# Optimization experiments

Measured on AMD Instinct MI355X. Metric: run time of the kernel, lower is better.

Reference implementation:

```python
import jax, jax.numpy as jnp
import numpy as np

TOP_K = 2
EPS = float(np.finfo(np.float64).eps)  # combine() clamps zeros to np.finfo(float).eps


def setup_inputs() -> dict:
    key = jax.random.key(0)
    ks = jax.random.split(key, 6)
    B, D, H, O, E = 2048, 1024, 2048, 512, 8
    return {
        "x": jax.random.normal(ks[0], (B, D), dtype=jnp.float32),
        "w_gate": jax.random.normal(ks[1], (D, E), dtype=jnp.float32) * 0.02,
        "fc1_w": jax.random.normal(ks[2], (E, D, H), dtype=jnp.float32) * 0.02,
        "fc1_b": jax.random.normal(ks[3], (E, H), dtype=jnp.float32) * 0.02,
        "fc2_w": jax.random.normal(ks[4], (E, H, O), dtype=jnp.float32) * 0.02,
        "fc2_b": jax.random.normal(ks[5], (E, O), dtype=jnp.float32) * 0.02,
    }


def _gates(x, w_gate):
    # Noisy top-k gating in eval mode (no noise): clean logits -> top-k -> softmax over top-k -> scatter.
    logits = x @ w_gate                              # [B, E]
    top_logits, top_idx = jax.lax.top_k(logits, TOP_K)  # [B, K]
    top_gates = jax.nn.softmax(top_logits, axis=-1)      # 'softmax' gating over selected experts
    B = x.shape[0]
    gates = jnp.zeros(logits.shape, logits.dtype)
    gates = gates.at[jnp.arange(B)[:, None], top_idx].set(top_gates)
    return gates                                      # [B, E], zero for non-selected experts


def reference(x, w_gate, fc1_w, fc1_b, fc2_w, fc2_b):
    gates = _gates(x, w_gate)                         # [B, E]
    # Dense-equivalent of SparseDispatcher: non-selected experts have gate 0,
    # so weighting by gates reproduces dispatch/expert/combine exactly.
    h = jax.nn.gelu(jnp.einsum('bd,edh->ebh', x, fc1_w) + fc1_b[:, None, :],
                    approximate=False)                # [E, B, H]
    logp = jax.nn.log_softmax(jnp.einsum('ebh,eho->ebo', h, fc2_w) + fc2_b[:, None, :],
                              axis=-1)                # [E, B, O] (MLP ends with LogSoftmax)
    # combine: sum_e gates[b,e] * exp(logp_e[b]), clamp zeros to eps, then log
    combined = jnp.einsum('ebo,be->bo', jnp.exp(logp), gates)  # [B, O]
    combined = jnp.where(combined == 0, jnp.asarray(EPS, combined.dtype), combined)
    return jnp.log(combined)
```

## Files before the change

### kernel.cpp

```cpp
#include <hip/hip_runtime.h>
#include <stdint.h>

#define Bn 2048
#define Dn 1024
#define Hn 2048
#define On 512
#define En 8

typedef __bf16 bf16x8 __attribute__((ext_vector_type(8)));
typedef float f32x4 __attribute__((ext_vector_type(4)));
typedef unsigned short ushort_t;
typedef ushort_t ushort8v __attribute__((ext_vector_type(8)));

__device__ __forceinline__ ushort_t f2bf(float v) {
  union { float f; uint32_t u; } a; a.f = v;
  uint32_t u = a.u;
  return (ushort_t)((u + 0x7fffu + ((u >> 16) & 1u)) >> 16);
}

__device__ __forceinline__ void gload16(const void* g, void* l) {
  __builtin_amdgcn_global_load_lds((const uint32_t*)g, (uint32_t*)l, 16, 0, 0);
}

__global__ void init_kernel(int* counts, int* cursors) {
  int t = threadIdx.x;
  if (t < En) { counts[t] = 0; cursors[t] = 0; }
}

#define NB_G (Bn / 8)
#define NB_T1 ((Dn / 64) * (Hn / 64) * En)
#define NB_T2 ((Hn / 64) * (On / 64) * En)

__device__ __forceinline__ void tcast64(const float* __restrict__ inp, ushort_t* __restrict__ outp,
                                        int R, int C, int r0, int c0, float* tile ) {
  int t = threadIdx.x;
  int rr = t >> 4;
  int cc4 = (t & 15) * 4;
#pragma unroll
  for (int j = 0; j < 4; j++) {
    float4 v = *(const float4*)&inp[(size_t)(r0 + j * 16 + rr) * C + c0 + cc4];
    float* tp = &tile[(j * 16 + rr) * 65 + cc4];
    tp[0] = v.x; tp[1] = v.y; tp[2] = v.z; tp[3] = v.w;
  }
  __syncthreads();
  int orow = t >> 2, g = t & 3;
  ushort8v o0, o1;
#pragma unroll
  for (int i = 0; i < 8; i++) o0[i] = f2bf(tile[(g * 16 + i) * 65 + orow]);
#pragma unroll
  for (int i = 0; i < 8; i++) o1[i] = f2bf(tile[(g * 16 + 8 + i) * 65 + orow]);
  ushort_t* op = &outp[(size_t)(c0 + orow) * R + r0 + g * 16];
  *(ushort8v*)op = o0;
  *(ushort8v*)(op + 8) = o1;
}

__global__ __launch_bounds__(256) void prep_kernel(
    const float* __restrict__ x, const float* __restrict__ wg,
    const float* __restrict__ fc1w, const float* __restrict__ fc2w,
    ushort_t* __restrict__ x_bf, ushort_t* __restrict__ w1t, ushort_t* __restrict__ w2t,
    int* __restrict__ top_idx, float* __restrict__ gates, int* __restrict__ counts) {
  __shared__ float smem[En * Dn];
  __shared__ int lcnt[En];
  int bid = blockIdx.x;
  int t = threadIdx.x;

  if (bid < NB_G) {
    float* wgs = smem;
    for (int i = t; i < Dn * En; i += 256) {
      int d = i >> 3, e = i & 7;
      wgs[e * Dn + d] = wg[i];
    }
    if (t < En) lcnt[t] = 0;
    __syncthreads();
    int w = t >> 6, lane = t & 63;
#pragma unroll
    for (int r = 0; r < 2; r++) {
      int b = bid * 8 + w * 2 + r;
      const float* xr = x + (size_t)b * Dn;
      ushort_t* xo = x_bf + (size_t)b * Dn;
      float xv[16];
#pragma unroll
      for (int j = 0; j < 16; j++) xv[j] = xr[lane + j * 64];
      float acc[En];
#pragma unroll
      for (int e = 0; e < En; e++) acc[e] = 0.f;
#pragma unroll
      for (int j = 0; j < 16; j++) {
        int d = lane + j * 64;
        xo[d] = f2bf(xv[j]);
#pragma unroll
        for (int e = 0; e < En; e++) acc[e] += xv[j] * wgs[e * Dn + d];
      }
#pragma unroll
      for (int off = 32; off; off >>= 1) {
#pragma unroll
        for (int e = 0; e < En; e++) acc[e] += __shfl_down(acc[e], off);
      }
      if (lane == 0) {
        float best = -1e30f, second = -1e30f; int bi = 0, si = 0;
#pragma unroll
        for (int e = 0; e < En; e++) {
          float l = acc[e];
          if (l > best) { second = best; si = bi; best = l; bi = e; }
          else if (l > second) { second = l; si = e; }
        }
        float e1 = expf(second - best);
        float inv = 1.f / (1.f + e1);
        top_idx[2 * b] = bi; top_idx[2 * b + 1] = si;
        gates[2 * b] = inv;  gates[2 * b + 1] = e1 * inv;
        atomicAdd(&lcnt[bi], 1);
        atomicAdd(&lcnt[si], 1);
      }
    }
    __syncthreads();
    if (t < En) {
      int c = lcnt[t];
      if (c) atomicAdd(&counts[t], c);
    }
  } else if (bid < NB_G + NB_T1) {
    int idx = bid - NB_G;
    constexpr int TPE = (Dn / 64) * (Hn / 64);
    int z = idx / TPE, rem = idx % TPE;
    int r0 = (rem / (Hn / 64)) * 64, c0 = (rem % (Hn / 64)) * 64;
    tcast64(fc1w + (size_t)z * Dn * Hn, w1t + (size_t)z * Dn * Hn, Dn, Hn, r0, c0, smem);
  } else {
    int idx = bid - NB_G - NB_T1;
    constexpr int TPE = (Hn / 64) * (On / 64);
    int z = idx / TPE, rem = idx % TPE;
    int r0 = (rem / (On / 64)) * 64, c0 = (rem % (On / 64)) * 64;
    tcast64(fc2w + (size_t)z * Hn * On, w2t + (size_t)z * Hn * On, Hn, On, r0, c0, smem);
  }
}

__global__ void offsets_kernel(const int* counts, int* offsets, int* cursors) {
  if (threadIdx.x == 0) {
    int s = 0;
    for (int e = 0; e < En; e++) { offsets[e] = s; s += counts[e]; }
  }
  if (threadIdx.x < En) cursors[threadIdx.x] = 0;
}

__global__ void assign_kernel(const int* __restrict__ top_idx, const int* __restrict__ offsets,
                              int* cursors, int* __restrict__ s2r, int* __restrict__ r2s) {
  int b = blockIdx.x * 256 + threadIdx.x;
  if (b >= Bn) return;
#pragma unroll
  for (int k = 0; k < 2; k++) {
    int e = top_idx[2 * b + k];
    int pos = atomicAdd(&cursors[e], 1);
    int slot = offsets[e] + pos;
    s2r[slot] = b;
    r2s[2 * b + k] = slot;
  }
}

template <bool GATHER, bool FC1, int N, int K, int SPLITK>
__global__ __launch_bounds__(256, 8) void moe_gemm_kernel(
    const ushort_t* __restrict__ A, const ushort_t* __restrict__ WT,
    const float* __restrict__ bias, const int* __restrict__ offsets,
    const int* __restrict__ counts, const int* __restrict__ s2r,
    ushort_t* __restrict__ outH, float* __restrict__ outL, float* __restrict__ outL2) {
  constexpr int NBL = N / 64;
  constexpr int KS = K / SPLITK;
  constexpr int NT = KS / 64;
  int e = blockIdx.z;
  int cnt = counts[e];
  int rb = blockIdx.y;
  if (rb * 64 >= cnt) return;
  int base = offsets[e];
  int ks = blockIdx.x / NBL;
  int nb = (blockIdx.x % NBL) * 64;
  int k0 = ks * KS;
  __shared__ __align__(16) ushort_t As[64 * 64];
  __shared__ __align__(16) ushort_t Bs[64 * 64];
  int t = threadIdx.x;
  int lane = t & 63, w = t >> 6;
  int wr = w >> 1, wc = w & 1;

  int srow = t >> 3;
  int scol = ((t & 7) ^ (srow & 7)) * 8;

  const ushort_t* aptr[2];
#pragma unroll
  for (int i = 0; i < 2; i++) {
    int lr = rb * 64 + i * 32 + srow;
    int lrc = lr < cnt ? lr : cnt - 1;
    int slot = base + lrc;
    int row = GATHER ? s2r[slot] : slot;
    aptr[i] = A + (size_t)row * K + k0 + scol;
  }
  const ushort_t* bptr = WT + ((size_t)e * N + nb + srow) * K + k0 + scol;

  f32x4 zero = {0.f, 0.f, 0.f, 0.f};
  f32x4 acc[2][2];
#pragma unroll
  for (int m = 0; m < 2; m++)
#pragma unroll
    for (int n = 0; n < 2; n++) acc[m][n] = zero;

  int a_r = wr * 32 + (lane & 15);
  int b_r = wc * 32 + (lane & 15);
  int axor = lane & 7;
  int c16 = lane >> 4;

  for (int kt = 0; kt < NT; kt++) {
#pragma unroll
    for (int i = 0; i < 2; i++) gload16(aptr[i] + kt * 64, &As[i * 2048 + t * 8]);
#pragma unroll
    for (int i = 0; i < 2; i++)
      gload16(bptr + (size_t)i * 32 * K + kt * 64, &Bs[i * 2048 + t * 8]);
    __syncthreads();
#pragma unroll
    for (int kk = 0; kk < 2; kk++) {
      bf16x8 af[2], bfr[2];
#pragma unroll
      for (int m = 0; m < 2; m++)
        af[m] = *(const bf16x8*)((const char*)As + (a_r + m * 16) * 128 +
                                 (((kk * 4 + c16) ^ axor) << 4));
#pragma unroll
      for (int n = 0; n < 2; n++)
        bfr[n] = *(const bf16x8*)((const char*)Bs + (b_r + n * 16) * 128 +
                                  (((kk * 4 + c16) ^ axor) << 4));
#pragma unroll
      for (int m = 0; m < 2; m++)
#pragma unroll
        for (int n = 0; n < 2; n++)
          acc[m][n] = __builtin_amdgcn_mfma_f32_16x16x32_bf16(af[m], bfr[n], acc[m][n], 0, 0, 0);
    }
    __syncthreads();
  }

  float* dst = (SPLITK > 1 && ks > 0) ? (outL2 + (size_t)(ks - 1) * (2 * Bn * On)) : outL;
  int lr0 = rb * 64 + wr * 32;
#pragma unroll
  for (int m = 0; m < 2; m++) {
#pragma unroll
    for (int i = 0; i < 4; i++) {
      int lr = lr0 + m * 16 + (lane >> 4) * 4 + i;
      if (lr < cnt) {
        int slot = base + lr;
#pragma unroll
        for (int n = 0; n < 2; n++) {
          int col = nb + wc * 32 + n * 16 + (lane & 15);
          float v = acc[m][n][i] + (ks == 0 ? bias[e * N + col] : 0.f);
          if (FC1) {
            float g = 0.5f * v * (1.0f + erff(v * 0.70710678118654752f));
            outH[(size_t)slot * N + col] = f2bf(g);
          } else {
            dst[(size_t)slot * N + col] = v;
          }
        }
      }
    }
  }
}

__device__ __forceinline__ float blk_reduce(float v, bool ismax) {
  __shared__ float sbuf[4];
  int lane = threadIdx.x & 63, w = threadIdx.x >> 6;
#pragma unroll
  for (int off = 32; off; off >>= 1) {
    float o = __shfl_down(v, off);
    v = ismax ? fmaxf(v, o) : (v + o);
  }
  __syncthreads();
  if (lane == 0) sbuf[w] = v;
  __syncthreads();
  float r = sbuf[0];
#pragma unroll
  for (int i = 1; i < 4; i++) r = ismax ? fmaxf(r, sbuf[i]) : (r + sbuf[i]);
  return r;
}

__global__ void combine_kernel(const float* __restrict__ l2a, const float* __restrict__ l2b,
                               const int* __restrict__ r2s, const float* __restrict__ gates,
                               float* __restrict__ out) {
  int b = blockIdx.x, t = threadIdx.x;
  float c0 = 0.f, c1 = 0.f;
#pragma unroll
  for (int k = 0; k < 2; k++) {
    int slot = r2s[2 * b + k];
    float g = gates[2 * b + k];
    const float* lp0 = l2a + (size_t)slot * On;
    const float* lp1 = l2b + (size_t)slot * On;
    float v0 = lp0[t] + lp1[t];
    float v1 = lp0[t + 256] + lp1[t + 256];
    float m = blk_reduce(fmaxf(v0, v1), true);
    float s = blk_reduce(expf(v0 - m) + expf(v1 - m), false);
    float lse = m + logf(s);
    c0 += g * expf(v0 - lse);
    c1 += g * expf(v1 - lse);
  }
  const float EPSv = 2.220446049250313e-16f;
  out[(size_t)b * On + t] = logf(fmaxf(c0, EPSv));
  out[(size_t)b * On + t + 256] = logf(fmaxf(c1, EPSv));
}

extern "C" void kernel_launch(void* const* d_in, const int* in_sizes, int n_in,
                              void* d_out, int out_size, void* d_ws, size_t ws_size,
                              hipStream_t stream) {
  const float* x = (const float*)d_in[0];
  const float* wgate = (const float*)d_in[1];
  const float* fc1w = (const float*)d_in[2];
  const float* fc1b = (const float*)d_in[3];
  const float* fc2w = (const float*)d_in[4];
  const float* fc2b = (const float*)d_in[5];
  float* out = (float*)d_out;

  char* ws = (char*)d_ws;
  size_t o = 0;
  ushort_t* x_bf = (ushort_t*)(ws + o); o += (size_t)Bn * Dn * 2;
  ushort_t* w1t  = (ushort_t*)(ws + o); o += (size_t)En * Hn * Dn * 2;
  ushort_t* w2t  = (ushort_t*)(ws + o); o += (size_t)En * On * Hn * 2;
  ushort_t* hbuf = (ushort_t*)(ws + o); o += (size_t)2 * Bn * Hn * 2;
  float* l2buf   = (float*)(ws + o);    o += (size_t)2 * Bn * On * 4;
  int* top_idx   = (int*)(ws + o);      o += (size_t)Bn * 2 * 4;
  float* gates   = (float*)(ws + o);    o += (size_t)Bn * 2 * 4;
  int* r2s       = (int*)(ws + o);      o += (size_t)Bn * 2 * 4;
  int* s2r       = (int*)(ws + o);      o += (size_t)2 * Bn * 4;
  int* counts    = (int*)(ws + o);      o += 64;
  int* offsets   = (int*)(ws + o);      o += 64;
  int* cursors   = (int*)(ws + o);      o += 64;
  float* l2buf1  = (float*)w1t;

  hipLaunchKernelGGL(init_kernel, dim3(1), dim3(64), 0, stream, counts, cursors);
  hipLaunchKernelGGL(prep_kernel, dim3(NB_G + NB_T1 + NB_T2), dim3(256), 0, stream,
                     x, wgate, fc1w, fc2w, x_bf, w1t, w2t, top_idx, gates, counts);
  hipLaunchKernelGGL(offsets_kernel, dim3(1), dim3(64), 0, stream, counts, offsets, cursors);
  hipLaunchKernelGGL(assign_kernel, dim3(Bn / 256), dim3(256), 0, stream,
                     top_idx, offsets, cursors, s2r, r2s);
  hipLaunchKernelGGL((moe_gemm_kernel<true, true, Hn, Dn, 1>), dim3(Hn / 64, 32, En), dim3(256),
                     0, stream, x_bf, w1t, fc1b, offsets, counts, s2r, hbuf, (float*)nullptr,
                     (float*)nullptr);
  hipLaunchKernelGGL((moe_gemm_kernel<false, false, On, Hn, 2>), dim3((On / 64) * 2, 32, En),
                     dim3(256), 0, stream, hbuf, w2t, fc2b, offsets, counts, s2r,
                     (ushort_t*)nullptr, l2buf, l2buf1);
  hipLaunchKernelGGL(combine_kernel, dim3(Bn), dim3(256), 0, stream, l2buf, l2buf1, r2s, gates, out);
}
```

Before: 131.6 us.

## Run fc1 expert GEMM in FP8 with scaled weights and separate x cast

New measurement: 124.9 us. 1.05x faster.

```diff
diff --git a/kernel.cpp b/kernel.cpp
--- a/kernel.cpp
+++ b/kernel.cpp
@@ -11,6 +11,7 @@
 typedef float f32x4 __attribute__((ext_vector_type(4)));
 typedef unsigned short ushort_t;
 typedef ushort_t ushort8v __attribute__((ext_vector_type(8)));
+typedef unsigned char u8;
 
 __device__ __forceinline__ ushort_t f2bf(float v) {
   union { float f; uint32_t u; } a; a.f = v;
@@ -22,20 +23,40 @@
   __builtin_amdgcn_global_load_lds((const uint32_t*)g, (uint32_t*)l, 16, 0, 0);
 }
 
+__device__ __forceinline__ int pk4_fp8(float a, float b, float c, float d) {
+  int w = __builtin_amdgcn_cvt_pk_fp8_f32(a, b, 0, false);
+  w = __builtin_amdgcn_cvt_pk_fp8_f32(c, d, w, true);
+  return w;
+}
+
 __global__ void init_kernel(int* counts, int* cursors) {
   int t = threadIdx.x;
   if (t < En) { counts[t] = 0; cursors[t] = 0; }
+}
+
+__global__ __launch_bounds__(256) void cast_x8_kernel(const float* __restrict__ in,
+                                                      u8* __restrict__ out) {
+  int i = blockIdx.x * 256 + threadIdx.x;
+  const float4* p = (const float4*)in + (size_t)i * 4;
+  float4 a = p[0], b = p[1], c = p[2], d = p[3];
+  int4 o;
+  o.x = pk4_fp8(a.x, a.y, a.z, a.w);
+  o.y = pk4_fp8(b.x, b.y, b.z, b.w);
+  o.z = pk4_fp8(c.x, c.y, c.z, c.w);
+  o.w = pk4_fp8(d.x, d.y, d.z, d.w);
+  *(int4*)(out + (size_t)i * 16) = o;
 }
 
 #define NB_G (Bn / 8)
 #define NB_T1 ((Dn / 64) * (Hn / 64) * En)
 #define NB_T2 ((Hn / 64) * (On / 64) * En)
-
-__device__ __forceinline__ void tcast64(const float* __restrict__ inp, ushort_t* __restrict__ outp,
-                                        int R, int C, int r0, int c0, float* tile ) {
-  int t = threadIdx.x;
-  int rr = t >> 4;
-  int cc4 = (t & 15) * 4;
+#define W1SCALE 64.0f
+
+__device__ __forceinline__ void tcast64_bf(const float* __restrict__ inp,
+                                           ushort_t* __restrict__ outp,
+                                           int R, int C, int r0, int c0, float* tile) {
+  int t = threadIdx.x;
+  int rr = t >> 4, cc4 = (t & 15) * 4;
 #pragma unroll
   for (int j = 0; j < 4; j++) {
     float4 v = *(const float4*)&inp[(size_t)(r0 + j * 16 + rr) * C + c0 + cc4];
@@ -54,10 +75,35 @@
   *(ushort8v*)(op + 8) = o1;
 }
 
+__device__ __forceinline__ void tcast64_f8(const float* __restrict__ inp,
+                                           u8* __restrict__ outp,
+                                           int R, int C, int r0, int c0, float* tile) {
+  int t = threadIdx.x;
+  int rr = t >> 4, cc4 = (t & 15) * 4;
+#pragma unroll
+  for (int j = 0; j < 4; j++) {
+    float4 v = *(const float4*)&inp[(size_t)(r0 + j * 16 + rr) * C + c0 + cc4];
+    float* tp = &tile[(j * 16 + rr) * 65 + cc4];
+    tp[0] = v.x; tp[1] = v.y; tp[2] = v.z; tp[3] = v.w;
+  }
+  __syncthreads();
+  int orow = t >> 2, g = t & 3;
+  int4 o;
+#pragma unroll
+  for (int q = 0; q < 4; q++) {
+    float v0 = tile[(g * 16 + q * 4 + 0) * 65 + orow] * W1SCALE;
+    float v1 = tile[(g * 16 + q * 4 + 1) * 65 + orow] * W1SCALE;
+    float v2 = tile[(g * 16 + q * 4 + 2) * 65 + orow] * W1SCALE;
+    float v3 = tile[(g * 16 + q * 4 + 3) * 65 + orow] * W1SCALE;
+    ((int*)&o)[q] = pk4_fp8(v0, v1, v2, v3);
+  }
+  *(int4*)&outp[(size_t)(c0 + orow) * R + r0 + g * 16] = o;
+}
+
 __global__ __launch_bounds__(256) void prep_kernel(
     const float* __restrict__ x, const float* __restrict__ wg,
     const float* __restrict__ fc1w, const float* __restrict__ fc2w,
-    ushort_t* __restrict__ x_bf, ushort_t* __restrict__ w1t, ushort_t* __restrict__ w2t,
+    u8* __restrict__ w1t8, ushort_t* __restrict__ w2t,
     int* __restrict__ top_idx, float* __restrict__ gates, int* __restrict__ counts) {
   __shared__ float smem[En * Dn];
   __shared__ int lcnt[En];
@@ -77,7 +123,6 @@
     for (int r = 0; r < 2; r++) {
       int b = bid * 8 + w * 2 + r;
       const float* xr = x + (size_t)b * Dn;
-      ushort_t* xo = x_bf + (size_t)b * Dn;
       float xv[16];
 #pragma unroll
       for (int j = 0; j < 16; j++) xv[j] = xr[lane + j * 64];
@@ -87,7 +132,6 @@
 #pragma unroll
       for (int j = 0; j < 16; j++) {
         int d = lane + j * 64;
-        xo[d] = f2bf(xv[j]);
 #pragma unroll
         for (int e = 0; e < En; e++) acc[e] += xv[j] * wgs[e * Dn + d];
       }
@@ -122,13 +166,13 @@
     constexpr int TPE = (Dn / 64) * (Hn / 64);
     int z = idx / TPE, rem = idx % TPE;
     int r0 = (rem / (Hn / 64)) * 64, c0 = (rem % (Hn / 64)) * 64;
-    tcast64(fc1w + (size_t)z * Dn * Hn, w1t + (size_t)z * Dn * Hn, Dn, Hn, r0, c0, smem);
+    tcast64_f8(fc1w + (size_t)z * Dn * Hn, w1t8 + (size_t)z * Dn * Hn, Dn, Hn, r0, c0, smem);
   } else {
     int idx = bid - NB_G - NB_T1;
     constexpr int TPE = (Hn / 64) * (On / 64);
     int z = idx / TPE, rem = idx % TPE;
     int r0 = (rem / (On / 64)) * 64, c0 = (rem % (On / 64)) * 64;
-    tcast64(fc2w + (size_t)z * Hn * On, w2t + (size_t)z * Hn * On, Hn, On, r0, c0, smem);
+    tcast64_bf(fc2w + (size_t)z * Hn * On, w2t + (size_t)z * Hn * On, Hn, On, r0, c0, smem);
   }
 }
 
@@ -154,12 +198,98 @@
   }
 }
 
-template <bool GATHER, bool FC1, int N, int K, int SPLITK>
-__global__ __launch_bounds__(256, 8) void moe_gemm_kernel(
+__global__ __launch_bounds__(256, 8) void fc1_fp8_kernel(
+    const u8* __restrict__ A, const u8* __restrict__ WT,
+    const float* __restrict__ bias, const int* __restrict__ offsets,
+    const int* __restrict__ counts, const int* __restrict__ s2r,
+    ushort_t* __restrict__ outH) {
+  constexpr int K = Dn;
+  constexpr int NT = K / 64;
+  int e = blockIdx.z;
+  int cnt = counts[e];
+  int rb = blockIdx.y;
+  if (rb * 64 >= cnt) return;
+  int base = offsets[e];
+  int nb = blockIdx.x * 64;
+  __shared__ __align__(16) u8 As[64 * 64];
+  __shared__ __align__(16) u8 Bs[64 * 64];
+  int t = threadIdx.x;
+  int lane = t & 63, w = t >> 6;
+  int wr = w >> 1, wc = w & 1;
+
+  int srow = t >> 2;
+  int sslot = (t & 3) ^ ((srow >> 1) & 3);
+  int scol = sslot * 16;
+
+  int lr = rb * 64 + srow;
+  int lrc = lr < cnt ? lr : cnt - 1;
+  const u8* aptr = A + (size_t)s2r[base + lrc] * K + scol;
+  const u8* bptr = WT + ((size_t)e * Hn + nb + srow) * K + scol;
+
+  f32x4 zero = {0.f, 0.f, 0.f, 0.f};
+  f32x4 acc[2][2];
+#pragma unroll
+  for (int m = 0; m < 2; m++)
+#pragma unroll
+    for (int n = 0; n < 2; n++) acc[m][n] = zero;
+
+  int a_r = wr * 32 + (lane & 15);
+  int b_r = wc * 32 + (lane & 15);
+  int rkey = ((lane & 15) >> 1) & 3;
+  int slb = (lane >> 4) >> 1;
+  int half = ((lane >> 4) & 1) * 8;
+
+  for (int kt = 0; kt < NT; kt++) {
+    gload16(aptr + kt * 64, &As[t * 16]);
+    gload16(bptr + kt * 64, &Bs[t * 16]);
+    __syncthreads();
+#pragma unroll
+    for (int kk = 0; kk < 2; kk++) {
+      long af[2], bfr[2];
+#pragma unroll
+      for (int m = 0; m < 2; m++)
+        af[m] = *(const long*)(As + (a_r + m * 16) * 64 +
+                               (((kk * 2 + slb) ^ rkey) << 4) + half);
+#pragma unroll
+      for (int n = 0; n < 2; n++)
+        bfr[n] = *(const long*)(Bs + (b_r + n * 16) * 64 +
+                                (((kk * 2 + slb) ^ rkey) << 4) + half);
+#pragma unroll
+      for (int m = 0; m < 2; m++)
+#pragma unroll
+        for (int n = 0; n < 2; n++)
+          acc[m][n] = __builtin_amdgcn_mfma_f32_16x16x32_fp8_fp8(af[m], bfr[n], acc[m][n], 0, 0, 0);
+    }
+    __syncthreads();
+  }
+
+  const float INV = 1.0f / W1SCALE;
+  int lr0 = rb * 64 + wr * 32;
+#pragma unroll
+  for (int m = 0; m < 2; m++) {
+#pragma unroll
+    for (int i = 0; i < 4; i++) {
+      int orow = lr0 + m * 16 + (lane >> 4) * 4 + i;
+      if (orow < cnt) {
+        int slot = base + orow;
+#pragma unroll
+        for (int n = 0; n < 2; n++) {
+          int col = nb + wc * 32 + n * 16 + (lane & 15);
+          float v = acc[m][n][i] * INV + bias[e * Hn + col];
+          float g = 0.5f * v * (1.0f + erff(v * 0.70710678118654752f));
+          outH[(size_t)slot * Hn + col] = f2bf(g);
+        }
+      }
+    }
+  }
+}
+
+template <int N, int K, int SPLITK>
+__global__ __launch_bounds__(256, 8) void fc2_gemm_kernel(
     const ushort_t* __restrict__ A, const ushort_t* __restrict__ WT,
     const float* __restrict__ bias, const int* __restrict__ offsets,
-    const int* __restrict__ counts, const int* __restrict__ s2r,
-    ushort_t* __restrict__ outH, float* __restrict__ outL, float* __restrict__ outL2) {
+    const int* __restrict__ counts,
+    float* __restrict__ outL, float* __restrict__ outL2) {
   constexpr int NBL = N / 64;
   constexpr int KS = K / SPLITK;
   constexpr int NT = KS / 64;
@@ -185,9 +315,7 @@
   for (int i = 0; i < 2; i++) {
     int lr = rb * 64 + i * 32 + srow;
     int lrc = lr < cnt ? lr : cnt - 1;
-    int slot = base + lrc;
-    int row = GATHER ? s2r[slot] : slot;
-    aptr[i] = A + (size_t)row * K + k0 + scol;
+    aptr[i] = A + (size_t)(base + lrc) * K + k0 + scol;
   }
   const ushort_t* bptr = WT + ((size_t)e * N + nb + srow) * K + k0 + scol;
 
@@ -230,7 +358,7 @@
     __syncthreads();
   }
 
-  float* dst = (SPLITK > 1 && ks > 0) ? (outL2 + (size_t)(ks - 1) * (2 * Bn * On)) : outL;
+  float* dst = (ks > 0) ? outL2 : outL;
   int lr0 = rb * 64 + wr * 32;
 #pragma unroll
   for (int m = 0; m < 2; m++) {
@@ -243,12 +371,7 @@
         for (int n = 0; n < 2; n++) {
           int col = nb + wc * 32 + n * 16 + (lane & 15);
           float v = acc[m][n][i] + (ks == 0 ? bias[e * N + col] : 0.f);
-          if (FC1) {
-            float g = 0.5f * v * (1.0f + erff(v * 0.70710678118654752f));
-            outH[(size_t)slot * N + col] = f2bf(g);
-          } else {
-            dst[(size_t)slot * N + col] = v;
-          }
+          dst[(size_t)slot * N + col] = v;
         }
       }
     }
@@ -309,8 +432,8 @@
 
   char* ws = (char*)d_ws;
   size_t o = 0;
-  ushort_t* x_bf = (ushort_t*)(ws + o); o += (size_t)Bn * Dn * 2;
-  ushort_t* w1t  = (ushort_t*)(ws + o); o += (size_t)En * Hn * Dn * 2;
+  u8* x_f8       = (u8*)(ws + o);       o += (size_t)Bn * Dn;
+  u8* w1t8       = (u8*)(ws + o);       o += (size_t)En * Hn * Dn;
   ushort_t* w2t  = (ushort_t*)(ws + o); o += (size_t)En * On * Hn * 2;
   ushort_t* hbuf = (ushort_t*)(ws + o); o += (size_t)2 * Bn * Hn * 2;
   float* l2buf   = (float*)(ws + o);    o += (size_t)2 * Bn * On * 4;
@@ -321,19 +444,18 @@
   int* counts    = (int*)(ws + o);      o += 64;
   int* offsets   = (int*)(ws + o);      o += 64;
   int* cursors   = (int*)(ws + o);      o += 64;
-  float* l2buf1  = (float*)w1t;
+  float* l2buf1  = (float*)w1t8;
 
   hipLaunchKernelGGL(init_kernel, dim3(1), dim3(64), 0, stream, counts, cursors);
+  hipLaunchKernelGGL(cast_x8_kernel, dim3(Bn * Dn / 16 / 256), dim3(256), 0, stream, x, x_f8);
   hipLaunchKernelGGL(prep_kernel, dim3(NB_G + NB_T1 + NB_T2), dim3(256), 0, stream,
-                     x, wgate, fc1w, fc2w, x_bf, w1t, w2t, top_idx, gates, counts);
+                     x, wgate, fc1w, fc2w, w1t8, w2t, top_idx, gates, counts);
   hipLaunchKernelGGL(offsets_kernel, dim3(1), dim3(64), 0, stream, counts, offsets, cursors);
   hipLaunchKernelGGL(assign_kernel, dim3(Bn / 256), dim3(256), 0, stream,
                      top_idx, offsets, cursors, s2r, r2s);
-  hipLaunchKernelGGL((moe_gemm_kernel<true, true, Hn, Dn, 1>), dim3(Hn / 64, 32, En), dim3(256),
-                     0, stream, x_bf, w1t, fc1b, offsets, counts, s2r, hbuf, (float*)nullptr,
-                     (float*)nullptr);
-  hipLaunchKernelGGL((moe_gemm_kernel<false, false, On, Hn, 2>), dim3((On / 64) * 2, 32, En),
-                     dim3(256), 0, stream, hbuf, w2t, fc2b, offsets, counts, s2r,
-                     (ushort_t*)nullptr, l2buf, l2buf1);
+  hipLaunchKernelGGL(fc1_fp8_kernel, dim3(Hn / 64, 32, En), dim3(256), 0, stream,
+                     x_f8, w1t8, fc1b, offsets, counts, s2r, hbuf);
+  hipLaunchKernelGGL((fc2_gemm_kernel<On, Hn, 2>), dim3((On / 64) * 2, 32, En), dim3(256),
+                     0, stream, hbuf, w2t, fc2b, offsets, counts, l2buf, l2buf1);
   hipLaunchKernelGGL(combine_kernel, dim3(Bn), dim3(256), 0, stream, l2buf, l2buf1, r2s, gates, out);
 }
```

## Switch expert GEMMs from bf16 to fp8 with scaled weights

Applied to the files above, without the earlier changes.

Measured after the change: 115.2 us. -12.4%, faster.

```diff
diff --git a/kernel.cpp b/kernel.cpp
--- a/kernel.cpp
+++ b/kernel.cpp
@@ -7,10 +7,9 @@
 #define On 512
 #define En 8
 
-typedef __bf16 bf16x8 __attribute__((ext_vector_type(8)));
 typedef float f32x4 __attribute__((ext_vector_type(4)));
 typedef unsigned short ushort_t;
-typedef ushort_t ushort8v __attribute__((ext_vector_type(8)));
+typedef unsigned char u8;
 
 __device__ __forceinline__ ushort_t f2bf(float v) {
   union { float f; uint32_t u; } a; a.f = v;
@@ -22,20 +21,45 @@
   __builtin_amdgcn_global_load_lds((const uint32_t*)g, (uint32_t*)l, 16, 0, 0);
 }
 
+__device__ __forceinline__ int pk4_fp8(float a, float b, float c, float d) {
+  int w = __builtin_amdgcn_cvt_pk_fp8_f32(a, b, 0, false);
+  w = __builtin_amdgcn_cvt_pk_fp8_f32(c, d, w, true);
+  return w;
+}
+
+__device__ __forceinline__ u8 f2fp8(float v) {
+  int w = __builtin_amdgcn_cvt_pk_fp8_f32(v, v, 0, false);
+  return (u8)(w & 0xff);
+}
+
 __global__ void init_kernel(int* counts, int* cursors) {
   int t = threadIdx.x;
   if (t < En) { counts[t] = 0; cursors[t] = 0; }
 }
 
+__global__ __launch_bounds__(256) void cast_x8_kernel(const float* __restrict__ in,
+                                                      u8* __restrict__ out) {
+  int i = blockIdx.x * 256 + threadIdx.x;
+  const float4* p = (const float4*)in + (size_t)i * 4;
+  float4 a = p[0], b = p[1], c = p[2], d = p[3];
+  int4 o;
+  o.x = pk4_fp8(a.x, a.y, a.z, a.w);
+  o.y = pk4_fp8(b.x, b.y, b.z, b.w);
+  o.z = pk4_fp8(c.x, c.y, c.z, c.w);
+  o.w = pk4_fp8(d.x, d.y, d.z, d.w);
+  *(int4*)(out + (size_t)i * 16) = o;
+}
+
 #define NB_G (Bn / 8)
 #define NB_T1 ((Dn / 64) * (Hn / 64) * En)
 #define NB_T2 ((Hn / 64) * (On / 64) * En)
-
-__device__ __forceinline__ void tcast64(const float* __restrict__ inp, ushort_t* __restrict__ outp,
-                                        int R, int C, int r0, int c0, float* tile ) {
+#define WSCALE 64.0f
+
+__device__ __forceinline__ void tcast64_f8(const float* __restrict__ inp,
+                                           u8* __restrict__ outp,
+                                           int R, int C, int r0, int c0, float* tile) {
   int t = threadIdx.x;
-  int rr = t >> 4;
-  int cc4 = (t & 15) * 4;
+  int rr = t >> 4, cc4 = (t & 15) * 4;
 #pragma unroll
   for (int j = 0; j < 4; j++) {
     float4 v = *(const float4*)&inp[(size_t)(r0 + j * 16 + rr) * C + c0 + cc4];
@@ -44,20 +68,22 @@
   }
   __syncthreads();
   int orow = t >> 2, g = t & 3;
-  ushort8v o0, o1;
-#pragma unroll
-  for (int i = 0; i < 8; i++) o0[i] = f2bf(tile[(g * 16 + i) * 65 + orow]);
-#pragma unroll
-  for (int i = 0; i < 8; i++) o1[i] = f2bf(tile[(g * 16 + 8 + i) * 65 + orow]);
-  ushort_t* op = &outp[(size_t)(c0 + orow) * R + r0 + g * 16];
-  *(ushort8v*)op = o0;
-  *(ushort8v*)(op + 8) = o1;
+  int4 o;
+#pragma unroll
+  for (int q = 0; q < 4; q++) {
+    float v0 = tile[(g * 16 + q * 4 + 0) * 65 + orow] * WSCALE;
+    float v1 = tile[(g * 16 + q * 4 + 1) * 65 + orow] * WSCALE;
+    float v2 = tile[(g * 16 + q * 4 + 2) * 65 + orow] * WSCALE;
+    float v3 = tile[(g * 16 + q * 4 + 3) * 65 + orow] * WSCALE;
+    ((int*)&o)[q] = pk4_fp8(v0, v1, v2, v3);
+  }
+  *(int4*)&outp[(size_t)(c0 + orow) * R + r0 + g * 16] = o;
 }
 
 __global__ __launch_bounds__(256) void prep_kernel(
     const float* __restrict__ x, const float* __restrict__ wg,
     const float* __restrict__ fc1w, const float* __restrict__ fc2w,
-    ushort_t* __restrict__ x_bf, ushort_t* __restrict__ w1t, ushort_t* __restrict__ w2t,
+    u8* __restrict__ w1t8, u8* __restrict__ w2t8,
     int* __restrict__ top_idx, float* __restrict__ gates, int* __restrict__ counts) {
   __shared__ float smem[En * Dn];
   __shared__ int lcnt[En];
@@ -77,7 +103,6 @@
     for (int r = 0; r < 2; r++) {
       int b = bid * 8 + w * 2 + r;
       const float* xr = x + (size_t)b * Dn;
-      ushort_t* xo = x_bf + (size_t)b * Dn;
       float xv[16];
 #pragma unroll
       for (int j = 0; j < 16; j++) xv[j] = xr[lane + j * 64];
@@ -87,7 +112,6 @@
 #pragma unroll
       for (int j = 0; j < 16; j++) {
         int d = lane + j * 64;
-        xo[d] = f2bf(xv[j]);
 #pragma unroll
         for (int e = 0; e < En; e++) acc[e] += xv[j] * wgs[e * Dn + d];
       }
@@ -122,13 +146,13 @@
     constexpr int TPE = (Dn / 64) * (Hn / 64);
     int z = idx / TPE, rem = idx % TPE;
     int r0 = (rem / (Hn / 64)) * 64, c0 = (rem % (Hn / 64)) * 64;
-    tcast64(fc1w + (size_t)z * Dn * Hn, w1t + (size_t)z * Dn * Hn, Dn, Hn, r0, c0, smem);
+    tcast64_f8(fc1w + (size_t)z * Dn * Hn, w1t8 + (size_t)z * Dn * Hn, Dn, Hn, r0, c0, smem);
   } else {
     int idx = bid - NB_G - NB_T1;
     constexpr int TPE = (Hn / 64) * (On / 64);
     int z = idx / TPE, rem = idx % TPE;
     int r0 = (rem / (On / 64)) * 64, c0 = (rem % (On / 64)) * 64;
-    tcast64(fc2w + (size_t)z * Hn * On, w2t + (size_t)z * Hn * On, Hn, On, r0, c0, smem);
+    tcast64_f8(fc2w + (size_t)z * Hn * On, w2t8 + (size_t)z * Hn * On, Hn, On, r0, c0, smem);
   }
 }
 
@@ -154,12 +178,12 @@
   }
 }
 
-template <bool GATHER, bool FC1, int N, int K, int SPLITK>
-__global__ __launch_bounds__(256, 8) void moe_gemm_kernel(
-    const ushort_t* __restrict__ A, const ushort_t* __restrict__ WT,
+template <bool FC1, int N, int K, int SPLITK>
+__global__ __launch_bounds__(256, 8) void fp8_gemm_kernel(
+    const u8* __restrict__ A, const u8* __restrict__ WT,
     const float* __restrict__ bias, const int* __restrict__ offsets,
     const int* __restrict__ counts, const int* __restrict__ s2r,
-    ushort_t* __restrict__ outH, float* __restrict__ outL, float* __restrict__ outL2) {
+    u8* __restrict__ outH8, float* __restrict__ outL, float* __restrict__ outL2) {
   constexpr int NBL = N / 64;
   constexpr int KS = K / SPLITK;
   constexpr int NT = KS / 64;
@@ -171,25 +195,20 @@
   int ks = blockIdx.x / NBL;
   int nb = (blockIdx.x % NBL) * 64;
   int k0 = ks * KS;
-  __shared__ __align__(16) ushort_t As[64 * 64];
-  __shared__ __align__(16) ushort_t Bs[64 * 64];
+  __shared__ __align__(16) u8 As[64 * 64];
+  __shared__ __align__(16) u8 Bs[64 * 64];
   int t = threadIdx.x;
   int lane = t & 63, w = t >> 6;
   int wr = w >> 1, wc = w & 1;
 
-  int srow = t >> 3;
-  int scol = ((t & 7) ^ (srow & 7)) * 8;
-
-  const ushort_t* aptr[2];
-#pragma unroll
-  for (int i = 0; i < 2; i++) {
-    int lr = rb * 64 + i * 32 + srow;
-    int lrc = lr < cnt ? lr : cnt - 1;
-    int slot = base + lrc;
-    int row = GATHER ? s2r[slot] : slot;
-    aptr[i] = A + (size_t)row * K + k0 + scol;
-  }
-  const ushort_t* bptr = WT + ((size_t)e * N + nb + srow) * K + k0 + scol;
+  int srow = t >> 2;
+  int sslot = (t & 3) ^ ((srow >> 1) & 3);
+  int scol = sslot * 16;
+
+  int lr = rb * 64 + srow;
+  int lrc = lr < cnt ? lr : cnt - 1;
+  const u8* aptr = A + (size_t)(FC1 ? s2r[base + lrc] : (base + lrc)) * K + k0 + scol;
+  const u8* bptr = WT + ((size_t)e * N + nb + srow) * K + k0 + scol;
 
   f32x4 zero = {0.f, 0.f, 0.f, 0.f};
   f32x4 acc[2][2];
@@ -200,53 +219,53 @@
 
   int a_r = wr * 32 + (lane & 15);
   int b_r = wc * 32 + (lane & 15);
-  int axor = lane & 7;
-  int c16 = lane >> 4;
+  int rkey = ((lane & 15) >> 1) & 3;
+  int slb = (lane >> 4) >> 1;
+  int half = ((lane >> 4) & 1) * 8;
 
   for (int kt = 0; kt < NT; kt++) {
-#pragma unroll
-    for (int i = 0; i < 2; i++) gload16(aptr[i] + kt * 64, &As[i * 2048 + t * 8]);
-#pragma unroll
-    for (int i = 0; i < 2; i++)
-      gload16(bptr + (size_t)i * 32 * K + kt * 64, &Bs[i * 2048 + t * 8]);
+    gload16(aptr + kt * 64, &As[t * 16]);
+    gload16(bptr + kt * 64, &Bs[t * 16]);
     __syncthreads();
 #pragma unroll
     for (int kk = 0; kk < 2; kk++) {
-      bf16x8 af[2], bfr[2];
+      long af[2], bfr[2];
 #pragma unroll
       for (int m = 0; m < 2; m++)
-        af[m] = *(const bf16x8*)((const char*)As + (a_r + m * 16) * 128 +
-                                 (((kk * 4 + c16) ^ axor) << 4));
+        af[m] = *(const long*)(As + (a_r + m * 16) * 64 +
+                               (((kk * 2 + slb) ^ rkey) << 4) + half);
 #pragma unroll
       for (int n = 0; n < 2; n++)
-        bfr[n] = *(const bf16x8*)((const char*)Bs + (b_r + n * 16) * 128 +
-                                  (((kk * 4 + c16) ^ axor) << 4));
+        bfr[n] = *(const long*)(Bs + (b_r + n * 16) * 64 +
+                                (((kk * 2 + slb) ^ rkey) << 4) + half);
 #pragma unroll
       for (int m = 0; m < 2; m++)
 #pragma unroll
         for (int n = 0; n < 2; n++)
-          acc[m][n] = __builtin_amdgcn_mfma_f32_16x16x32_bf16(af[m], bfr[n], acc[m][n], 0, 0, 0);
+          acc[m][n] = __builtin_amdgcn_mfma_f32_16x16x32_fp8_fp8(af[m], bfr[n], acc[m][n], 0, 0, 0);
     }
     __syncthreads();
   }
 
-  float* dst = (SPLITK > 1 && ks > 0) ? (outL2 + (size_t)(ks - 1) * (2 * Bn * On)) : outL;
+  const float INV = 1.0f / WSCALE;
+  float* dst = (SPLITK > 1 && ks > 0) ? outL2 : outL;
   int lr0 = rb * 64 + wr * 32;
 #pragma unroll
   for (int m = 0; m < 2; m++) {
 #pragma unroll
     for (int i = 0; i < 4; i++) {
-      int lr = lr0 + m * 16 + (lane >> 4) * 4 + i;
-      if (lr < cnt) {
-        int slot = base + lr;
+      int orow = lr0 + m * 16 + (lane >> 4) * 4 + i;
+      if (orow < cnt) {
+        int slot = base + orow;
 #pragma unroll
         for (int n = 0; n < 2; n++) {
           int col = nb + wc * 32 + n * 16 + (lane & 15);
-          float v = acc[m][n][i] + (ks == 0 ? bias[e * N + col] : 0.f);
           if (FC1) {
+            float v = acc[m][n][i] * INV + bias[e * N + col];
             float g = 0.5f * v * (1.0f + erff(v * 0.70710678118654752f));
-            outH[(size_t)slot * N + col] = f2bf(g);
+            outH8[(size_t)slot * N + col] = f2fp8(g);
           } else {
+            float v = acc[m][n][i] * INV + (ks == 0 ? bias[e * N + col] : 0.f);
             dst[(size_t)slot * N + col] = v;
           }
         }
@@ -309,31 +328,32 @@
 
   char* ws = (char*)d_ws;
   size_t o = 0;
-  ushort_t* x_bf = (ushort_t*)(ws + o); o += (size_t)Bn * Dn * 2;
-  ushort_t* w1t  = (ushort_t*)(ws + o); o += (size_t)En * Hn * Dn * 2;
-  ushort_t* w2t  = (ushort_t*)(ws + o); o += (size_t)En * On * Hn * 2;
-  ushort_t* hbuf = (ushort_t*)(ws + o); o += (size_t)2 * Bn * Hn * 2;
-  float* l2buf   = (float*)(ws + o);    o += (size_t)2 * Bn * On * 4;
-  int* top_idx   = (int*)(ws + o);      o += (size_t)Bn * 2 * 4;
-  float* gates   = (float*)(ws + o);    o += (size_t)Bn * 2 * 4;
-  int* r2s       = (int*)(ws + o);      o += (size_t)Bn * 2 * 4;
-  int* s2r       = (int*)(ws + o);      o += (size_t)2 * Bn * 4;
-  int* counts    = (int*)(ws + o);      o += 64;
-  int* offsets   = (int*)(ws + o);      o += 64;
-  int* cursors   = (int*)(ws + o);      o += 64;
-  float* l2buf1  = (float*)w1t;
+  u8* x_f8     = (u8*)(ws + o);    o += (size_t)Bn * Dn;
+  u8* w1t8     = (u8*)(ws + o);    o += (size_t)En * Hn * Dn;
+  u8* w2t8     = (u8*)(ws + o);    o += (size_t)En * On * Hn;
+  u8* hbuf8    = (u8*)(ws + o);    o += (size_t)2 * Bn * Hn;
+  float* l2buf = (float*)(ws + o); o += (size_t)2 * Bn * On * 4;
+  int* top_idx = (int*)(ws + o);   o += (size_t)Bn * 2 * 4;
+  float* gates = (float*)(ws + o); o += (size_t)Bn * 2 * 4;
+  int* r2s     = (int*)(ws + o);   o += (size_t)Bn * 2 * 4;
+  int* s2r     = (int*)(ws + o);   o += (size_t)2 * Bn * 4;
+  int* counts  = (int*)(ws + o);   o += 64;
+  int* offsets = (int*)(ws + o);   o += 64;
+  int* cursors = (int*)(ws + o);   o += 64;
+  float* l2buf1 = (float*)w1t8;
 
   hipLaunchKernelGGL(init_kernel, dim3(1), dim3(64), 0, stream, counts, cursors);
+  hipLaunchKernelGGL(cast_x8_kernel, dim3(Bn * Dn / 16 / 256), dim3(256), 0, stream, x, x_f8);
   hipLaunchKernelGGL(prep_kernel, dim3(NB_G + NB_T1 + NB_T2), dim3(256), 0, stream,
-                     x, wgate, fc1w, fc2w, x_bf, w1t, w2t, top_idx, gates, counts);
+                     x, wgate, fc1w, fc2w, w1t8, w2t8, top_idx, gates, counts);
   hipLaunchKernelGGL(offsets_kernel, dim3(1), dim3(64), 0, stream, counts, offsets, cursors);
   hipLaunchKernelGGL(assign_kernel, dim3(Bn / 256), dim3(256), 0, stream,
                      top_idx, offsets, cursors, s2r, r2s);
-  hipLaunchKernelGGL((moe_gemm_kernel<true, true, Hn, Dn, 1>), dim3(Hn / 64, 32, En), dim3(256),
-                     0, stream, x_bf, w1t, fc1b, offsets, counts, s2r, hbuf, (float*)nullptr,
-                     (float*)nullptr);
-  hipLaunchKernelGGL((moe_gemm_kernel<false, false, On, Hn, 2>), dim3((On / 64) * 2, 32, En),
-                     dim3(256), 0, stream, hbuf, w2t, fc2b, offsets, counts, s2r,
-                     (ushort_t*)nullptr, l2buf, l2buf1);
+  hipLaunchKernelGGL((fp8_gemm_kernel<true, Hn, Dn, 1>), dim3(Hn / 64, 32, En), dim3(256),
+                     0, stream, x_f8, w1t8, fc1b, offsets, counts, s2r, hbuf8,
+                     (float*)nullptr, (float*)nullptr);
+  hipLaunchKernelGGL((fp8_gemm_kernel<false, On, Hn, 2>), dim3((On / 64) * 2, 32, En), dim3(256),
+                     0, stream, hbuf8, w2t8, fc2b, offsets, counts, s2r, (u8*)nullptr,
+                     l2buf, l2buf1);
   hipLaunchKernelGGL(combine_kernel, dim3(Bn), dim3(256), 0, stream, l2buf, l2buf1, r2s, gates, out);
 }
```
